# Optimization experiments

Hardware: AMD Instinct MI355X
Metric: run time of the kernel (lower is better)

The kernel has to match this reference:

```python
import jax, jax.numpy as jnp
import numpy as np


def _fft_feats(x):
    # x: [B, 3, H, W] float32
    B, C, H, W = x.shape
    gray = 0.299 * x[:, 0] + 0.587 * x[:, 1] + 0.114 * x[:, 2]  # [B,H,W]
    mag = jnp.abs(jnp.fft.fftshift(jnp.fft.fft2(gray), axes=(-2, -1))) + 1e-8
    mag = mag / (mag.max(axis=(-2, -1), keepdims=True) + 1e-8)
    m = mag.reshape(B, -1)
    n = m.shape[1]
    mean = m.mean(axis=1)
    std = jnp.clip(jnp.std(m, axis=1, ddof=1), 1e-8, None)  # torch unbiased std
    mx = m.max(axis=1)
    mn = m.min(axis=1)
    gt_mean = (m > mean[:, None]).astype(jnp.float32).mean(axis=1)
    # torch.median returns the lower of the two middle values for even n
    med = jnp.sort(m, axis=1)[:, (n - 1) // 2]
    q1 = mag[:, : H // 4].mean(axis=(1, 2))
    q2 = mag[:, H // 4 : H // 2].mean(axis=(1, 2))
    q3 = mag[:, H // 2 : 3 * H // 4].mean(axis=(1, 2))
    q4 = mag[:, 3 * H // 4 :].mean(axis=(1, 2))
    gt_half = (m > 0.5).astype(jnp.float32).mean(axis=1)
    gt_tenth = (m > 0.1).astype(jnp.float32).mean(axis=1)
    feats = jnp.stack([mean, std, mx, mn, gt_mean, med, q1, q2, q3, q4, gt_half, gt_tenth], axis=1)
    return jnp.clip(feats, -10.0, 10.0)  # [B,12]


def _bn(h, gamma, beta):
    # BatchNorm1d, training-mode forward (batch statistics, biased var), eps=1e-5
    mu = h.mean(axis=0)
    var = h.var(axis=0)
    return gamma * (h - mu) / jnp.sqrt(var + 1e-5) + beta


def _mlp(f, W1, b1, g1, be1, W2, b2, g2, be2, W3, b3):
    h = jax.nn.relu(_bn(f @ W1 + b1, g1, be1))  # Dropout(0.1) treated as identity (eval)
    h = jax.nn.relu(_bn(h @ W2 + b2, g2, be2))
    return h @ W3 + b3


def setup_inputs() -> dict:
    key = jax.random.key(0)
    ks = jax.random.split(key, 8)
    B, H, W = 64, 512, 512
    D = 512  # output_dim
    x = jax.random.normal(ks[0], (B, 3, H, W), dtype=jnp.float32)
    W1 = jax.random.normal(ks[1], (12, 64), dtype=jnp.float32) * 0.2
    b1 = jnp.zeros((64,), jnp.float32)
    g1 = jnp.ones((64,), jnp.float32)
    be1 = jnp.zeros((64,), jnp.float32)
    W2 = jax.random.normal(ks[2], (64, 128), dtype=jnp.float32) * 0.1
    b2 = jnp.zeros((128,), jnp.float32)
    g2 = jnp.ones((128,), jnp.float32)
    be2 = jnp.zeros((128,), jnp.float32)
    W3 = jax.random.normal(ks[3], (128, D), dtype=jnp.float32) * 0.08
    b3 = jnp.zeros((D,), jnp.float32)
    return {"x": x, "W1": W1, "b1": b1, "g1": g1, "be1": be1,
            "W2": W2, "b2": b2, "g2": g2, "be2": be2, "W3": W3, "b3": b3}


def reference(x, W1, b1, g1, be1, W2, b2, g2, be2, W3, b3):
    feats = _fft_feats(x)
    return _mlp(feats, W1, b1, g1, be1, W2, b2, g2, be2, W3, b3)
```

## Files before the change

kernel.cpp:

```cpp
#include <hip/hip_runtime.h>
#include <math.h>

#ifndef M_PI
#define M_PI 3.14159265358979323846
#endif

#define BB 64
#define HH 512
#define WW 512
#define NPIX (HH*WW)
#define MED_K 131072u
#define WS 260
#define PADI(i) ((i) + ((i) >> 5))

__device__ __forceinline__ float2 cmulf(float2 a, float2 b){
  return make_float2(a.x*b.x - a.y*b.y, a.x*b.y + a.y*b.x);
}
__device__ __forceinline__ unsigned rev9(unsigned v){ return __brev(v) >> 23; }

__device__ __forceinline__ float wredf(float v){
  #pragma unroll
  for (int o = 32; o > 0; o >>= 1) v += __shfl_down(v, o, 64);
  return v;
}
__device__ __forceinline__ float wred_min(float v){
  #pragma unroll
  for (int o = 32; o > 0; o >>= 1) v = fminf(v, __shfl_down(v, o, 64));
  return v;
}
__device__ __forceinline__ float wred_max(float v){
  #pragma unroll
  for (int o = 32; o > 0; o >>= 1) v = fmaxf(v, __shfl_down(v, o, 64));
  return v;
}
__device__ __forceinline__ unsigned wred_addu(unsigned v){
  #pragma unroll
  for (int o = 32; o > 0; o >>= 1) v += __shfl_down(v, o, 64);
  return v;
}
__device__ __forceinline__ float wred_add_all(float v){
  #pragma unroll
  for (int o = 32; o > 0; o >>= 1) v += __shfl_xor(v, o, 64);
  return v;
}

__global__ void init_kernel(float2* __restrict__ twg, unsigned* __restrict__ scal){
  int t = threadIdx.x;
  double a = -2.0 * M_PI * (double)t / 512.0;
  twg[t] = make_float2((float)cos(a), (float)sin(a));
  #pragma unroll
  for (int q = 0; q < 8; ++q){
    int w = t*8 + q;
    scal[w] = (w >= 64 && w < 128) ? 0xFFFFFFFFu : 0u;
  }
}

__global__ __launch_bounds__(256) void row_fft_kernel(const float* __restrict__ x,
                                                      const float2* __restrict__ twg,
                                                      float2* __restrict__ out){
  __shared__ float sre[528], sim[528];
  __shared__ float2 tw[256];
  int t = threadIdx.x;
  tw[t] = twg[t];
  int pair = blockIdx.x;
  int b = pair >> 8, hp = pair & 255;
  const float* base = x + (size_t)b*3*NPIX + (size_t)(2*hp)*WW;
  int rsel = t >> 7;
  int f4i = t & 127;
  const float* rowbase = base + rsel*WW;
  float4 rv = ((const float4*)rowbase)[f4i];
  float4 gv = ((const float4*)(rowbase + NPIX))[f4i];
  float4 bv = ((const float4*)(rowbase + 2*NPIX))[f4i];
  float g[4] = {0.299f*rv.x + 0.587f*gv.x + 0.114f*bv.x,
                0.299f*rv.y + 0.587f*gv.y + 0.114f*bv.y,
                0.299f*rv.z + 0.587f*gv.z + 0.114f*bv.z,
                0.299f*rv.w + 0.587f*gv.w + 0.114f*bv.w};
  int col0 = f4i << 2;
  #pragma unroll
  for (int q = 0; q < 4; ++q){
    int p = PADI((int)rev9((unsigned)(col0 + q)));
    if (rsel == 0) sre[p] = g[q]; else sim[p] = g[q];
  }
  __syncthreads();
  #pragma unroll
  for (int st = 1; st <= 9; ++st){
    int half = 1 << (st-1);
    int k = t & (half - 1);
    int i1 = ((t >> (st-1)) << st) + k;
    int i2 = i1 + half;
    int p1 = PADI(i1), p2 = PADI(i2);
    float2 w = tw[k << (9 - st)];
    float2 u = make_float2(sre[p1], sim[p1]);
    float2 raw = make_float2(sre[p2], sim[p2]);
    float2 v = cmulf(w, raw);
    sre[p1] = u.x + v.x; sim[p1] = u.y + v.y;
    sre[p2] = u.x - v.x; sim[p2] = u.y - v.y;
    __syncthreads();
  }
  int row0 = (b << 9) + 2*hp;
  float2* o0 = out + (size_t)row0*WW;
  float2* o1 = o0 + WW;
  #pragma unroll
  for (int kk = 0; kk < 2; ++kk){
    int k = t + (kk << 8);
    if (k > 256) continue;
    int mk = (512 - k) & 511;
    int pk = PADI(k), pmk = PADI(mk);
    float zr = sre[pk], zi = sim[pk];
    float wr = sre[pmk], wi = sim[pmk];
    o0[k] = make_float2(0.5f*(zr + wr), 0.5f*(zi - wi));
    o1[k] = make_float2(0.5f*(zi + wi), 0.5f*(wr - zr));
  }
}

__global__ __launch_bounds__(512) void col_fft_kernel(const float2* __restrict__ in,
    const float2* __restrict__ twg,
    float* __restrict__ magc,
    unsigned* __restrict__ dmax, unsigned* __restrict__ dmin,
    double* __restrict__ sum, double* __restrict__ sumsq, double* __restrict__ qsum,
    unsigned* __restrict__ hist1)
{
  __shared__ float2 s[512*16];
  __shared__ float2 tw[256];
  __shared__ unsigned hs[256];
  __shared__ float buff[8][8];
  int t = threadIdx.x;
  if (t < 256){ tw[t] = twg[t]; hs[t] = 0u; }
  int b = blockIdx.x / 17;
  int j0 = (blockIdx.x % 17) << 4;
  const float2* base = in + (size_t)b*NPIX;
  for (int idx = t; idx < 512*16; idx += 512){
    int e = idx >> 4, c = idx & 15;
    int j = j0 + c;
    float2 v = (j <= 256) ? base[(size_t)e*WW + j] : make_float2(0.f, 0.f);
    s[(int)rev9((unsigned)e)*16 + c] = v;
  }
  __syncthreads();
  #pragma unroll
  for (int st = 1; st <= 9; ++st){
    int half = 1 << (st-1);
    #pragma unroll
    for (int qq = 0; qq < 8; ++qq){
      int tt = t + (qq << 9);
      int c = tt & 15;
      int kk = tt >> 4;
      int k = kk & (half - 1);
      int i1 = ((kk >> (st-1)) << st) + k;
      int i2 = i1 + half;
      float2 w = tw[k << (9 - st)];
      float2 u = s[i1*16 + c];
      float2 v = cmulf(w, s[i2*16 + c]);
      s[i1*16 + c] = make_float2(u.x + v.x, u.y + v.y);
      s[i2*16 + c] = make_float2(u.x - v.x, u.y - v.y);
    }
    __syncthreads();
  }
  float lsum=0.f, lsq=0.f, lq0=0.f, lq1=0.f, lq2=0.f, lq3=0.f;
  float lmn = 3.4e38f, lmx = 0.f;
  int wv = t >> 6, lane = t & 63;
  float* mo = magc + (size_t)b*(512*WS);
  for (int idx = t; idx < 512*16; idx += 512){
    int e = idx >> 4, c = idx & 15;
    int j = j0 + c;
    bool valid = (j <= 256);
    float2 v = s[e*16 + c];
    float m = sqrtf(v.x*v.x + v.y*v.y) + 1e-8f;
    int si = (e + 256) & 511;
    unsigned w = valid ? ((j == 0 || j == 256) ? 1u : 2u) : 0u;
    if (valid){
      mo[(size_t)si*WS + j] = m;
      float wm = (w == 2u) ? m + m : m;
      lsum += wm;
      lsq = fmaf(wm, m, lsq);
      lmn = fminf(lmn, m); lmx = fmaxf(lmx, m);
      int qa = si >> 7;
      lq0 += (qa==0)?m:0.f; lq1 += (qa==1)?m:0.f; lq2 += (qa==2)?m:0.f; lq3 += (qa==3)?m:0.f;
      if (w == 2u){
        int qb = si ? 3 - ((si-1) >> 7) : 0;
        lq0 += (qb==0)?m:0.f; lq1 += (qb==1)?m:0.f; lq2 += (qb==2)?m:0.f; lq3 += (qb==3)?m:0.f;
      }
    }
    unsigned bin = __float_as_uint(m) >> 23;
    bool done = !valid;
    while (true){
      unsigned long long act = __ballot(!done);
      if (act == 0ull) break;
      int src = __ffsll(act) - 1;
      unsigned lbin = __shfl(bin, src, 64);
      bool match = (!done) && (bin == lbin);
      unsigned long long ma = __ballot(match);
      unsigned long long m2 = __ballot(match && (w == 2u));
      if (lane == src){
        unsigned add = (unsigned)__popcll(ma) + (unsigned)__popcll(m2);
        atomicAdd(&hs[lbin], add);
      }
      done = done || match;
    }
  }
  float r0 = wredf(lsum), r1 = wredf(lsq);
  float r2 = wredf(lq0), r3 = wredf(lq1), r4 = wredf(lq2), r5 = wredf(lq3);
  float fmn = wred_min(lmn), fmx = wred_max(lmx);
  if (lane == 0){
    buff[0][wv]=r0; buff[1][wv]=r1; buff[2][wv]=r2;
    buff[3][wv]=r3; buff[4][wv]=r4; buff[5][wv]=r5;
    buff[6][wv]=fmn; buff[7][wv]=fmx;
  }
  __syncthreads();
  if (t == 0){
    double s0=0,s1=0,s2=0,s3=0,s4=0,s5=0; float mn=3.4e38f, mx=0.f;
    for (int i = 0; i < 8; ++i){
      s0+=(double)buff[0][i]; s1+=(double)buff[1][i]; s2+=(double)buff[2][i];
      s3+=(double)buff[3][i]; s4+=(double)buff[4][i]; s5+=(double)buff[5][i];
      mn=fminf(mn,buff[6][i]); mx=fmaxf(mx,buff[7][i]);
    }
    atomicAdd(sum + b, s0);
    atomicAdd(sumsq + b, s1);
    atomicAdd(qsum + b*4 + 0, s2);
    atomicAdd(qsum + b*4 + 1, s3);
    atomicAdd(qsum + b*4 + 2, s4);
    atomicAdd(qsum + b*4 + 3, s5);
    atomicMin(dmin + b, __float_as_uint(mn));
    atomicMax(dmax + b, __float_as_uint(mx));
  }
  unsigned* hb = hist1 + (size_t)b*256;
  if (t < 256){
    unsigned c = hs[t];
    if (c) atomicAdd(&hb[t], c);
  }
}

__global__ __launch_bounds__(256) void pass2_kernel(const float4* __restrict__ magc4,
    const unsigned* __restrict__ hist1, const double* __restrict__ sum,
    const unsigned* __restrict__ dmax,
    unsigned* __restrict__ hist2, unsigned* __restrict__ cnt_gtm,
    unsigned* __restrict__ cnt_half, unsigned* __restrict__ cnt_tenth)
{
  __shared__ unsigned h[16384];
  __shared__ unsigned part[256];
  __shared__ unsigned rb[3][8];
  __shared__ unsigned s_sel;
  int t = threadIdx.x, b = blockIdx.x;
  for (int i = t; i < 16384; i += 256) h[i] = 0;
  const unsigned* hb1 = hist1 + (size_t)b*256;
  part[t] = hb1[t];
  __syncthreads();
  if (t == 0){
    unsigned target = MED_K, cum = 0; int bin = 0;
    for (; bin < 256; ++bin){ if (cum + part[bin] >= target) break; cum += part[bin]; }
    s_sel = (unsigned)bin;
  }
  __syncthreads();
  unsigned s1 = s_sel;
  float meanf = (float)(sum[b] / (double)NPIX);
  float d = __uint_as_float(dmax[b]) + 1e-8f;
  float th = 0.5f*d, tl = 0.1f*d;
  const float4* p = magc4 + (size_t)b*(512*(WS/4)) + (size_t)blockIdx.y*128*(WS/4);
  unsigned lgm = 0, lh = 0, lt = 0;
  for (int idx = t; idx < 128*(WS/4); idx += 256){
    float4 v = p[idx];
    int k = idx % (WS/4);
    int jc0 = k*4;
    float a[4] = {v.x, v.y, v.z, v.w};
    #pragma unroll
    for (int q = 0; q < 4; ++q){
      int jc = jc0 + q;
      if (jc > 256) continue;
      unsigned w = (jc == 0 || jc == 256) ? 1u : 2u;
      float m = a[q];
      unsigned bits = __float_as_uint(m);
      if ((bits >> 23) == s1) atomicAdd(&h[(bits >> 9) & 0x3fffu], w);
      lgm += (m > meanf) ? w : 0u;
      lh  += (m > th) ? w : 0u;
      lt  += (m > tl) ? w : 0u;
    }
  }
  int lane = t & 63, wv = t >> 6;
  unsigned g0 = wred_addu(lgm), g1 = wred_addu(lh), g2 = wred_addu(lt);
  if (lane == 0){ rb[0][wv]=g0; rb[1][wv]=g1; rb[2][wv]=g2; }
  __syncthreads();
  if (t == 0){
    unsigned a0=0,a1=0,a2=0;
    for (int i = 0; i < 4; ++i){ a0+=rb[0][i]; a1+=rb[1][i]; a2+=rb[2][i]; }
    atomicAdd(cnt_gtm + b, a0);
    atomicAdd(cnt_half + b, a1);
    atomicAdd(cnt_tenth + b, a2);
  }
  unsigned* hb = hist2 + (size_t)b*16384;
  for (int i = t; i < 16384; i += 256){
    unsigned c = h[i];
    if (c) atomicAdd(&hb[i], c);
  }
}

__global__ __launch_bounds__(256) void scan2_feats_kernel(
    const unsigned* __restrict__ hist1, const unsigned* __restrict__ hist2,
    const unsigned* __restrict__ dmax, const unsigned* __restrict__ dmin,
    const double* __restrict__ sum, const double* __restrict__ sumsq,
    const double* __restrict__ qsum,
    const unsigned* __restrict__ cnt_half, const unsigned* __restrict__ cnt_tenth,
    const unsigned* __restrict__ cnt_gtmean,
    float* __restrict__ feats)
{
  int b = blockIdx.x, t = threadIdx.x;
  __shared__ unsigned part[256];
  __shared__ unsigned s_sel, s_rem;
  const unsigned* hb1 = hist1 + (size_t)b*256;
  part[t] = hb1[t];
  __syncthreads();
  if (t == 0){
    unsigned target = MED_K, cum = 0; int bin = 0;
    for (; bin < 256; ++bin){ if (cum + part[bin] >= target) break; cum += part[bin]; }
    s_sel = (unsigned)bin; s_rem = target - cum;
  }
  __syncthreads();
  const unsigned* hb2 = hist2 + (size_t)b*16384;
  {
    unsigned sp = 0;
    for (int i = 0; i < 64; ++i) sp += hb2[t*64 + i];
    part[t] = sp;
  }
  __syncthreads();
  if (t == 0){
    unsigned target = s_rem, cum = 0; int seg = 0;
    for (; seg < 256; ++seg){ if (cum + part[seg] >= target) break; cum += part[seg]; }
    unsigned r = target - cum;
    int bin = seg*64;
    for (;; ++bin){ unsigned c = hb2[bin]; if (c >= r) break; r -= c; }
    unsigned medbits = (s_sel << 23) | ((unsigned)bin << 9) | 256u;
    float maxv = __uint_as_float(dmax[b]);
    float dd_f = maxv + 1e-8f;
    double dd = (double)dd_f;
    double n = (double)NPIX;
    double sm = sum[b] / dd;
    double sq = sumsq[b] / (dd*dd);
    double mean = sm / n;
    double var = (sq - sm*sm/n) / (n - 1.0);
    if (var < 0.0) var = 0.0;
    float stdv = (float)sqrt(var);
    if (stdv < 1e-8f) stdv = 1e-8f;
    float f[12];
    f[0] = (float)mean;
    f[1] = stdv;
    f[2] = maxv / dd_f;
    f[3] = __uint_as_float(dmin[b]) / dd_f;
    f[4] = (float)((double)cnt_gtmean[b] / n);
    f[5] = __uint_as_float(medbits) / dd_f;
    f[6] = (float)(qsum[b*4+0] / dd * (1.0/65536.0));
    f[7] = (float)(qsum[b*4+1] / dd * (1.0/65536.0));
    f[8] = (float)(qsum[b*4+2] / dd * (1.0/65536.0));
    f[9] = (float)(qsum[b*4+3] / dd * (1.0/65536.0));
    f[10] = (float)((double)cnt_half[b] / n);
    f[11] = (float)((double)cnt_tenth[b] / n);
    #pragma unroll
    for (int i = 0; i < 12; ++i)
      feats[b*12 + i] = fminf(fmaxf(f[i], -10.f), 10.f);
  }
}

__global__ __launch_bounds__(64) void mlp1_kernel(const float* __restrict__ feats,
    const float* __restrict__ W1, const float* __restrict__ b1,
    const float* __restrict__ g1, const float* __restrict__ be1,
    float* __restrict__ h1t)
{
  int c = blockIdx.x, r = threadIdx.x;
  float acc = b1[c];
  #pragma unroll
  for (int k = 0; k < 12; ++k) acc += feats[r*12 + k] * W1[k*64 + c];
  float mu = wred_add_all(acc) * (1.f/BB);
  float dv = acc - mu;
  float var = wred_add_all(dv*dv) * (1.f/BB);
  float scv = g1[c] / sqrtf(var + 1e-5f);
  float v = dv*scv + be1[c];
  h1t[c*BB + r] = v > 0.f ? v : 0.f;
}

__global__ __launch_bounds__(64) void mlp2_kernel(const float* __restrict__ h1t,
    const float* __restrict__ W2, const float* __restrict__ b2,
    const float* __restrict__ g2, const float* __restrict__ be2,
    float* __restrict__ h2t)
{
  int c = blockIdx.x, r = threadIdx.x;
  float acc = b2[c];
  #pragma unroll 4
  for (int k = 0; k < 64; ++k) acc += h1t[k*BB + r] * W2[k*128 + c];
  float mu = wred_add_all(acc) * (1.f/BB);
  float dv = acc - mu;
  float var = wred_add_all(dv*dv) * (1.f/BB);
  float scv = g2[c] / sqrtf(var + 1e-5f);
  float v = dv*scv + be2[c];
  h2t[c*BB + r] = v > 0.f ? v : 0.f;
}

__global__ __launch_bounds__(256) void mlp3_kernel(const float* __restrict__ h2t,
    const float* __restrict__ W3, const float* __restrict__ b3,
    float* __restrict__ out)
{
  int r = threadIdx.x & 63;
  int w = threadIdx.x >> 6;
  int c = blockIdx.x*4 + w;
  float acc = b3[c];
  #pragma unroll 4
  for (int k = 0; k < 128; ++k) acc += h2t[k*BB + r] * W3[k*512 + c];
  out[r*512 + c] = acc;
}

extern "C" void kernel_launch(void* const* d_in, const int* in_sizes, int n_in,
                              void* d_out, int out_size, void* d_ws, size_t ws_size,
                              hipStream_t stream) {
  (void)in_sizes; (void)n_in; (void)out_size; (void)ws_size;
  const float* x   = (const float*)d_in[0];
  const float* W1  = (const float*)d_in[1];
  const float* b1  = (const float*)d_in[2];
  const float* g1  = (const float*)d_in[3];
  const float* be1 = (const float*)d_in[4];
  const float* W2  = (const float*)d_in[5];
  const float* b2  = (const float*)d_in[6];
  const float* g2  = (const float*)d_in[7];
  const float* be2 = (const float*)d_in[8];
  const float* W3  = (const float*)d_in[9];
  const float* b3  = (const float*)d_in[10];
  float* out = (float*)d_out;

  char* ws = (char*)d_ws;
  float2* bufc = (float2*)ws;
  float*  magc = (float*)(ws + 134217728);
  unsigned* hist1 = (unsigned*)(ws + 134217728 + 34078720);
  unsigned* hist2 = (unsigned*)(ws + 168296448 + 65536);
  char* sc = ws + 168361984 + 4194304;
  unsigned* dmax      = (unsigned*)(sc + 0);
  unsigned* dmin      = (unsigned*)(sc + 256);
  double*   sum       = (double*)(sc + 512);
  double*   sumsq     = (double*)(sc + 1024);
  double*   qsum      = (double*)(sc + 1536);
  unsigned* cnt_half  = (unsigned*)(sc + 3584);
  unsigned* cnt_tenth = (unsigned*)(sc + 3840);
  unsigned* cnt_gtm   = (unsigned*)(sc + 4096);
  float*    feats     = (float*)(sc + 5120);
  float*    h1t       = (float*)(sc + 8192);
  float*    h2t       = (float*)(sc + 8192 + 16384);
  float2*   twg       = (float2*)(sc + 8192 + 16384 + 32768);

  hipMemsetAsync(hist1, 0, 65536 + 4194304, stream);

  init_kernel<<<1, 256, 0, stream>>>(twg, (unsigned*)sc);
  row_fft_kernel<<<BB*256, 256, 0, stream>>>(x, twg, bufc);
  col_fft_kernel<<<BB*17, 512, 0, stream>>>(bufc, twg, magc, dmax, dmin, sum, sumsq, qsum, hist1);
  pass2_kernel<<<dim3(BB, 4), 256, 0, stream>>>((const float4*)magc, hist1, sum, dmax,
      hist2, cnt_gtm, cnt_half, cnt_tenth);
  scan2_feats_kernel<<<BB, 256, 0, stream>>>(hist1, hist2, dmax, dmin, sum, sumsq, qsum,
      cnt_half, cnt_tenth, cnt_gtm, feats);
  mlp1_kernel<<<64, 64, 0, stream>>>(feats, W1, b1, g1, be1, h1t);
  mlp2_kernel<<<128, 64, 0, stream>>>(h1t, W2, b2, g2, be2, h2t);
  mlp3_kernel<<<128, 256, 0, stream>>>(h2t, W3, b3, out);
}
```

Baseline: 488.6 us.

## Compute row and column FFTs in registers with one wave per transform

Both the row and column 512-point FFTs are replaced by a register-resident wave-level FFT. Each lane holds 8 points, and the butterflies exchange data through cross-lane shuffles instead of shared memory with a block barrier per stage. The intermediate buffer is compacted to a stride of 264 complex values, and the launch grids change so each wave handles one row pair or one column. This removes the per-stage barriers and LDS traffic and shrinks the intermediate memory, at the cost of more register pressure and shuffle instructions.

```diff
diff --git a/kernel.cpp b/kernel.cpp
--- a/kernel.cpp
+++ b/kernel.cpp
@@ -11,12 +11,8 @@
 #define NPIX (HH*WW)
 #define MED_K 131072u
 #define WS 260
-#define PADI(i) ((i) + ((i) >> 5))
-
-__device__ __forceinline__ float2 cmulf(float2 a, float2 b){
-  return make_float2(a.x*b.x - a.y*b.y, a.x*b.y + a.y*b.x);
-}
-__device__ __forceinline__ unsigned rev9(unsigned v){ return __brev(v) >> 23; }
+#define BSTRIDE 264
+#define SS 520
 
 __device__ __forceinline__ float wredf(float v){
   #pragma unroll
@@ -55,61 +51,174 @@
   }
 }
 
+__device__ __forceinline__ void build_twid(float2* T, const float2* __restrict__ twg,
+                                           int t, int nthr){
+  for (int i = t; i < 510; i += nthr){
+    int v = i + 2;
+    int z = 31 - __clz(v);
+    T[i] = twg[(v - (1 << z)) << (8 - z)];
+  }
+}
+
+__device__ __forceinline__ void wave_fft512(float (&re)[8], float (&im)[8],
+                                            const float2* T, int lane){
+  {
+    const int d = 1;
+    bool hi = (lane & d) != 0;
+    #pragma unroll
+    for (int r = 0; r < 8; ++r){
+      float pre = __shfl_xor(re[r], d, 64);
+      float pim = __shfl_xor(im[r], d, 64);
+      float ur = hi ? pre : re[r], ui = hi ? pim : im[r];
+      float vr = hi ? re[r] : pre, vi = hi ? im[r] : pim;
+      re[r] = hi ? ur - vr : ur + vr;
+      im[r] = hi ? ui - vi : ui + vi;
+    }
+  }
+  #pragma unroll
+  for (int st = 2; st <= 6; ++st){
+    const int d = 1 << (st - 1);
+    float2 w = T[((1 << (st - 1)) - 2) + (lane & (d - 1))];
+    bool hi = (lane & d) != 0;
+    #pragma unroll
+    for (int r = 0; r < 8; ++r){
+      float pre = __shfl_xor(re[r], d, 64);
+      float pim = __shfl_xor(im[r], d, 64);
+      float ur = hi ? pre : re[r], ui = hi ? pim : im[r];
+      float rr = hi ? re[r] : pre, ri = hi ? im[r] : pim;
+      float vr = w.x*rr - w.y*ri;
+      float vi = w.x*ri + w.y*rr;
+      re[r] = hi ? ur - vr : ur + vr;
+      im[r] = hi ? ui - vi : ui + vi;
+    }
+  }
+  {
+    float2 w = T[62 + lane];
+    #pragma unroll
+    for (int r = 0; r < 8; r += 2){
+      float vr = w.x*re[r+1] - w.y*im[r+1];
+      float vi = w.x*im[r+1] + w.y*re[r+1];
+      float ur = re[r], ui = im[r];
+      re[r]   = ur + vr; im[r]   = ui + vi;
+      re[r+1] = ur - vr; im[r+1] = ui - vi;
+    }
+  }
+  {
+    float2 w0 = T[126 + lane];
+    float2 w1 = T[190 + lane];
+    #pragma unroll
+    for (int rb = 0; rb < 8; rb += 4){
+      {
+        float vr = w0.x*re[rb+2] - w0.y*im[rb+2];
+        float vi = w0.x*im[rb+2] + w0.y*re[rb+2];
+        float ur = re[rb], ui = im[rb];
+        re[rb]   = ur + vr; im[rb]   = ui + vi;
+        re[rb+2] = ur - vr; im[rb+2] = ui - vi;
+      }
+      {
+        float vr = w1.x*re[rb+3] - w1.y*im[rb+3];
+        float vi = w1.x*im[rb+3] + w1.y*re[rb+3];
+        float ur = re[rb+1], ui = im[rb+1];
+        re[rb+1] = ur + vr; im[rb+1] = ui + vi;
+        re[rb+3] = ur - vr; im[rb+3] = ui - vi;
+      }
+    }
+  }
+  {
+    #pragma unroll
+    for (int r = 0; r < 4; ++r){
+      float2 w = T[254 + 64*r + lane];
+      float vr = w.x*re[r+4] - w.y*im[r+4];
+      float vi = w.x*im[r+4] + w.y*re[r+4];
+      float ur = re[r], ui = im[r];
+      re[r]   = ur + vr; im[r]   = ui + vi;
+      re[r+4] = ur - vr; im[r+4] = ui - vi;
+    }
+  }
+}
+
 __global__ __launch_bounds__(256) void row_fft_kernel(const float* __restrict__ x,
                                                       const float2* __restrict__ twg,
                                                       float2* __restrict__ out){
-  __shared__ float sre[528], sim[528];
-  __shared__ float2 tw[256];
+  __shared__ float2 T[510];
   int t = threadIdx.x;
-  tw[t] = twg[t];
-  int pair = blockIdx.x;
+  build_twid(T, twg, t, 256);
+  __syncthreads();
+  int lane = t & 63, wv = t >> 6;
+  int pair = blockIdx.x*4 + wv;
   int b = pair >> 8, hp = pair & 255;
-  const float* base = x + (size_t)b*3*NPIX + (size_t)(2*hp)*WW;
-  int rsel = t >> 7;
-  int f4i = t & 127;
-  const float* rowbase = base + rsel*WW;
-  float4 rv = ((const float4*)rowbase)[f4i];
-  float4 gv = ((const float4*)(rowbase + NPIX))[f4i];
-  float4 bv = ((const float4*)(rowbase + 2*NPIX))[f4i];
-  float g[4] = {0.299f*rv.x + 0.587f*gv.x + 0.114f*bv.x,
-                0.299f*rv.y + 0.587f*gv.y + 0.114f*bv.y,
-                0.299f*rv.z + 0.587f*gv.z + 0.114f*bv.z,
-                0.299f*rv.w + 0.587f*gv.w + 0.114f*bv.w};
-  int col0 = f4i << 2;
-  #pragma unroll
-  for (int q = 0; q < 4; ++q){
-    int p = PADI((int)rev9((unsigned)(col0 + q)));
-    if (rsel == 0) sre[p] = g[q]; else sim[p] = g[q];
-  }
-  __syncthreads();
-  #pragma unroll
-  for (int st = 1; st <= 9; ++st){
-    int half = 1 << (st-1);
-    int k = t & (half - 1);
-    int i1 = ((t >> (st-1)) << st) + k;
-    int i2 = i1 + half;
-    int p1 = PADI(i1), p2 = PADI(i2);
-    float2 w = tw[k << (9 - st)];
-    float2 u = make_float2(sre[p1], sim[p1]);
-    float2 raw = make_float2(sre[p2], sim[p2]);
-    float2 v = cmulf(w, raw);
-    sre[p1] = u.x + v.x; sim[p1] = u.y + v.y;
-    sre[p2] = u.x - v.x; sim[p2] = u.y - v.y;
-    __syncthreads();
-  }
+  int K = (int)(__brev((unsigned)lane) >> 26);
+  int c0 = K << 3;
+  const float* p0 = x + (size_t)b*3*NPIX + (size_t)(2*hp)*WW + c0;
+  const float* p1 = p0 + WW;
+  float4 ra0 = *(const float4*)(p0);          float4 ra1 = *(const float4*)(p0+4);
+  float4 ga0 = *(const float4*)(p0+NPIX);     float4 ga1 = *(const float4*)(p0+NPIX+4);
+  float4 ba0 = *(const float4*)(p0+2*NPIX);   float4 ba1 = *(const float4*)(p0+2*NPIX+4);
+  float4 rb0 = *(const float4*)(p1);          float4 rb1 = *(const float4*)(p1+4);
+  float4 gb0 = *(const float4*)(p1+NPIX);     float4 gb1 = *(const float4*)(p1+NPIX+4);
+  float4 bb0 = *(const float4*)(p1+2*NPIX);   float4 bb1 = *(const float4*)(p1+2*NPIX+4);
+  float g0[8] = {0.299f*ra0.x + 0.587f*ga0.x + 0.114f*ba0.x,
+                 0.299f*ra0.y + 0.587f*ga0.y + 0.114f*ba0.y,
+                 0.299f*ra0.z + 0.587f*ga0.z + 0.114f*ba0.z,
+                 0.299f*ra0.w + 0.587f*ga0.w + 0.114f*ba0.w,
+                 0.299f*ra1.x + 0.587f*ga1.x + 0.114f*ba1.x,
+                 0.299f*ra1.y + 0.587f*ga1.y + 0.114f*ba1.y,
+                 0.299f*ra1.z + 0.587f*ga1.z + 0.114f*ba1.z,
+                 0.299f*ra1.w + 0.587f*ga1.w + 0.114f*ba1.w};
+  float g1[8] = {0.299f*rb0.x + 0.587f*gb0.x + 0.114f*bb0.x,
+                 0.299f*rb0.y + 0.587f*gb0.y + 0.114f*bb0.y,
+                 0.299f*rb0.z + 0.587f*gb0.z + 0.114f*bb0.z,
+                 0.299f*rb0.w + 0.587f*gb0.w + 0.114f*bb0.w,
+                 0.299f*rb1.x + 0.587f*gb1.x + 0.114f*bb1.x,
+                 0.299f*rb1.y + 0.587f*gb1.y + 0.114f*bb1.y,
+                 0.299f*rb1.z + 0.587f*gb1.z + 0.114f*bb1.z,
+                 0.299f*rb1.w + 0.587f*gb1.w + 0.114f*bb1.w};
+  float re[8], im[8];
+  re[0]=g0[0]; re[4]=g0[1]; re[2]=g0[2]; re[6]=g0[3];
+  re[1]=g0[4]; re[5]=g0[5]; re[3]=g0[6]; re[7]=g0[7];
+  im[0]=g1[0]; im[4]=g1[1]; im[2]=g1[2]; im[6]=g1[3];
+  im[1]=g1[4]; im[5]=g1[5]; im[3]=g1[6]; im[7]=g1[7];
+  wave_fft512(re, im, T, lane);
   int row0 = (b << 9) + 2*hp;
-  float2* o0 = out + (size_t)row0*WW;
-  float2* o1 = o0 + WW;
-  #pragma unroll
-  for (int kk = 0; kk < 2; ++kk){
-    int k = t + (kk << 8);
-    if (k > 256) continue;
-    int mk = (512 - k) & 511;
-    int pk = PADI(k), pmk = PADI(mk);
-    float zr = sre[pk], zi = sim[pk];
-    float wr = sre[pmk], wi = sim[pmk];
+  float2* o0 = out + (size_t)row0*BSTRIDE;
+  float2* o1 = o0 + BSTRIDE;
+  int srcl = (64 - lane) & 63;
+  float p4r = __shfl(re[4], srcl, 64), p4i = __shfl(im[4], srcl, 64);
+  float p5r = __shfl(re[5], srcl, 64), p5i = __shfl(im[5], srcl, 64);
+  float p6r = __shfl(re[6], srcl, 64), p6i = __shfl(im[6], srcl, 64);
+  float p7r = __shfl(re[7], srcl, 64), p7i = __shfl(im[7], srcl, 64);
+  bool l0 = (lane == 0);
+  {
+    float zr = re[0], zi = im[0];
+    float wr = l0 ? re[0] : p7r, wi = l0 ? im[0] : p7i;
+    o0[lane] = make_float2(0.5f*(zr + wr), 0.5f*(zi - wi));
+    o1[lane] = make_float2(0.5f*(zi + wi), 0.5f*(wr - zr));
+  }
+  {
+    float zr = re[1], zi = im[1];
+    float wr = l0 ? re[7] : p6r, wi = l0 ? im[7] : p6i;
+    int k = lane + 64;
     o0[k] = make_float2(0.5f*(zr + wr), 0.5f*(zi - wi));
     o1[k] = make_float2(0.5f*(zi + wi), 0.5f*(wr - zr));
+  }
+  {
+    float zr = re[2], zi = im[2];
+    float wr = l0 ? re[6] : p5r, wi = l0 ? im[6] : p5i;
+    int k = lane + 128;
+    o0[k] = make_float2(0.5f*(zr + wr), 0.5f*(zi - wi));
+    o1[k] = make_float2(0.5f*(zi + wi), 0.5f*(wr - zr));
+  }
+  {
+    float zr = re[3], zi = im[3];
+    float wr = l0 ? re[5] : p4r, wi = l0 ? im[5] : p4i;
+    int k = lane + 192;
+    o0[k] = make_float2(0.5f*(zr + wr), 0.5f*(zi - wi));
+    o1[k] = make_float2(0.5f*(zi + wi), 0.5f*(wr - zr));
+  }
+  if (l0){
+    float zr = re[4], zi = im[4];
+    o0[256] = make_float2(zr, 0.f);
+    o1[256] = make_float2(zi, 0.f);
   }
 }
 
@@ -120,95 +229,88 @@
     double* __restrict__ sum, double* __restrict__ sumsq, double* __restrict__ qsum,
     unsigned* __restrict__ hist1)
 {
-  __shared__ float2 s[512*16];
-  __shared__ float2 tw[256];
+  __shared__ float st_re[8*SS];
+  __shared__ float st_im[8*SS];
+  __shared__ float2 T[510];
   __shared__ unsigned hs[256];
   __shared__ float buff[8][8];
   int t = threadIdx.x;
-  if (t < 256){ tw[t] = twg[t]; hs[t] = 0u; }
-  int b = blockIdx.x / 17;
-  int j0 = (blockIdx.x % 17) << 4;
-  const float2* base = in + (size_t)b*NPIX;
-  for (int idx = t; idx < 512*16; idx += 512){
-    int e = idx >> 4, c = idx & 15;
-    int j = j0 + c;
-    float2 v = (j <= 256) ? base[(size_t)e*WW + j] : make_float2(0.f, 0.f);
-    s[(int)rev9((unsigned)e)*16 + c] = v;
-  }
-  __syncthreads();
-  #pragma unroll
-  for (int st = 1; st <= 9; ++st){
-    int half = 1 << (st-1);
-    #pragma unroll
-    for (int qq = 0; qq < 8; ++qq){
-      int tt = t + (qq << 9);
-      int c = tt & 15;
-      int kk = tt >> 4;
-      int k = kk & (half - 1);
-      int i1 = ((kk >> (st-1)) << st) + k;
-      int i2 = i1 + half;
-      float2 w = tw[k << (9 - st)];
-      float2 u = s[i1*16 + c];
-      float2 v = cmulf(w, s[i2*16 + c]);
-      s[i1*16 + c] = make_float2(u.x + v.x, u.y + v.y);
-      s[i2*16 + c] = make_float2(u.x - v.x, u.y - v.y);
-    }
-    __syncthreads();
-  }
-  float lsum=0.f, lsq=0.f, lq0=0.f, lq1=0.f, lq2=0.f, lq3=0.f;
-  float lmn = 3.4e38f, lmx = 0.f;
-  int wv = t >> 6, lane = t & 63;
-  float* mo = magc + (size_t)b*(512*WS);
-  for (int idx = t; idx < 512*16; idx += 512){
-    int e = idx >> 4, c = idx & 15;
-    int j = j0 + c;
-    bool valid = (j <= 256);
-    float2 v = s[e*16 + c];
-    float m = sqrtf(v.x*v.x + v.y*v.y) + 1e-8f;
-    int si = (e + 256) & 511;
-    unsigned w = valid ? ((j == 0 || j == 256) ? 1u : 2u) : 0u;
-    if (valid){
+  int lane = t & 63, wv = t >> 6;
+  build_twid(T, twg, t, 512);
+  if (t < 256) hs[t] = 0u;
+  int b = blockIdx.x / 33;
+  int j0 = (blockIdx.x % 33) << 3;
+  const float2* base = in + (size_t)b * (size_t)(512*BSTRIDE);
+  #pragma unroll
+  for (int it = 0; it < 8; ++it){
+    int idx = t + (it << 9);
+    int e = idx >> 3, jj = idx & 7;
+    float2 v = base[(size_t)e*BSTRIDE + j0 + jj];
+    int se = e ^ (e >> 3);
+    st_re[jj*SS + se] = v.x;
+    st_im[jj*SS + se] = v.y;
+  }
+  __syncthreads();
+  int j = j0 + wv;
+  if (j <= 256){
+    int K = (int)(__brev((unsigned)lane) >> 26);
+    const int rv3[8] = {0,4,2,6,1,5,3,7};
+    float re[8], im[8];
+    #pragma unroll
+    for (int r = 0; r < 8; ++r){
+      int e = 8*K + rv3[r];
+      int se = e ^ K;
+      re[r] = st_re[wv*SS + se];
+      im[r] = st_im[wv*SS + se];
+    }
+    wave_fft512(re, im, T, lane);
+    unsigned wu = (j == 0 || j == 256) ? 1u : 2u;
+    float* mo = magc + (size_t)b*(512*WS);
+    float lsum=0.f, lsq=0.f, lq0=0.f, lq1=0.f, lq2=0.f, lq3=0.f;
+    float lmn = 3.4e38f, lmx = 0.f;
+    #pragma unroll
+    for (int r = 0; r < 8; ++r){
+      float m = sqrtf(re[r]*re[r] + im[r]*im[r]) + 1e-8f;
+      int k = lane + 64*r;
+      int si = (k + 256) & 511;
       mo[(size_t)si*WS + j] = m;
-      float wm = (w == 2u) ? m + m : m;
+      float wm = (wu == 2u) ? m + m : m;
       lsum += wm;
       lsq = fmaf(wm, m, lsq);
       lmn = fminf(lmn, m); lmx = fmaxf(lmx, m);
       int qa = si >> 7;
       lq0 += (qa==0)?m:0.f; lq1 += (qa==1)?m:0.f; lq2 += (qa==2)?m:0.f; lq3 += (qa==3)?m:0.f;
-      if (w == 2u){
+      if (wu == 2u){
         int qb = si ? 3 - ((si-1) >> 7) : 0;
         lq0 += (qb==0)?m:0.f; lq1 += (qb==1)?m:0.f; lq2 += (qb==2)?m:0.f; lq3 += (qb==3)?m:0.f;
       }
-    }
-    unsigned bin = __float_as_uint(m) >> 23;
-    bool done = !valid;
-    while (true){
-      unsigned long long act = __ballot(!done);
-      if (act == 0ull) break;
-      int src = __ffsll(act) - 1;
-      unsigned lbin = __shfl(bin, src, 64);
-      bool match = (!done) && (bin == lbin);
-      unsigned long long ma = __ballot(match);
-      unsigned long long m2 = __ballot(match && (w == 2u));
-      if (lane == src){
-        unsigned add = (unsigned)__popcll(ma) + (unsigned)__popcll(m2);
-        atomicAdd(&hs[lbin], add);
+      unsigned bin = __float_as_uint(m) >> 23;
+      bool done = false;
+      while (true){
+        unsigned long long act = __ballot(!done);
+        if (act == 0ull) break;
+        int srcl = __ffsll(act) - 1;
+        unsigned lbin = __shfl(bin, srcl, 64);
+        bool match = (!done) && (bin == lbin);
+        unsigned long long mb = __ballot(match);
+        if (lane == srcl) atomicAdd(&hs[lbin], wu * (unsigned)__popcll(mb));
+        done = done || match;
       }
-      done = done || match;
-    }
-  }
-  float r0 = wredf(lsum), r1 = wredf(lsq);
-  float r2 = wredf(lq0), r3 = wredf(lq1), r4 = wredf(lq2), r5 = wredf(lq3);
-  float fmn = wred_min(lmn), fmx = wred_max(lmx);
-  if (lane == 0){
-    buff[0][wv]=r0; buff[1][wv]=r1; buff[2][wv]=r2;
-    buff[3][wv]=r3; buff[4][wv]=r4; buff[5][wv]=r5;
-    buff[6][wv]=fmn; buff[7][wv]=fmx;
-  }
-  __syncthreads();
+    }
+    float r0 = wredf(lsum), r1 = wredf(lsq);
+    float r2 = wredf(lq0), r3 = wredf(lq1), r4 = wredf(lq2), r5 = wredf(lq3);
+    float fmn = wred_min(lmn), fmx = wred_max(lmx);
+    if (lane == 0){
+      buff[0][wv]=r0; buff[1][wv]=r1; buff[2][wv]=r2;
+      buff[3][wv]=r3; buff[4][wv]=r4; buff[5][wv]=r5;
+      buff[6][wv]=fmn; buff[7][wv]=fmx;
+    }
+  }
+  __syncthreads();
+  int nact = 257 - j0; if (nact > 8) nact = 8;
   if (t == 0){
     double s0=0,s1=0,s2=0,s3=0,s4=0,s5=0; float mn=3.4e38f, mx=0.f;
-    for (int i = 0; i < 8; ++i){
+    for (int i = 0; i < nact; ++i){
       s0+=(double)buff[0][i]; s1+=(double)buff[1][i]; s2+=(double)buff[2][i];
       s3+=(double)buff[3][i]; s4+=(double)buff[4][i]; s5+=(double)buff[5][i];
       mn=fminf(mn,buff[6][i]); mx=fmaxf(mx,buff[7][i]);
@@ -443,8 +545,8 @@
   hipMemsetAsync(hist1, 0, 65536 + 4194304, stream);
 
   init_kernel<<<1, 256, 0, stream>>>(twg, (unsigned*)sc);
-  row_fft_kernel<<<BB*256, 256, 0, stream>>>(x, twg, bufc);
-  col_fft_kernel<<<BB*17, 512, 0, stream>>>(bufc, twg, magc, dmax, dmin, sum, sumsq, qsum, hist1);
+  row_fft_kernel<<<BB*64, 256, 0, stream>>>(x, twg, bufc);
+  col_fft_kernel<<<BB*33, 512, 0, stream>>>(bufc, twg, magc, dmax, dmin, sum, sumsq, qsum, hist1);
   pass2_kernel<<<dim3(BB, 4), 256, 0, stream>>>((const float4*)magc, hist1, sum, dmax,
       hist2, cnt_gtm, cnt_half, cnt_tenth);
   scan2_feats_kernel<<<BB, 256, 0, stream>>>(hist1, hist2, dmax, dmin, sum, sumsq, qsum,
```

After: 460.8 us. 5.7% less time.
